# Optimization experiments

Hardware: AMD Instinct MI355X
Metric: run time of the kernel (lower is better)

The kernel has to match this reference:

```python
import jax, jax.numpy as jnp
import numpy as np

N_NODES = 50000
DIM = 128
N_EDGES = 800000
N_UID = 4096
ORDER = 3
LN_EPS = 1e-5


def setup_inputs() -> dict:
    key = jax.random.key(0)
    ks = jax.random.split(key, 6)
    scale = 1.0 / np.sqrt(DIM)
    embedding = jax.random.normal(ks[0], (N_NODES, DIM), jnp.float32) * np.sqrt(2.0 / DIM)  # kaiming-ish
    W = jax.random.normal(ks[1], (ORDER, DIM, DIM), jnp.float32) * scale
    b = jnp.zeros((ORDER, DIM), jnp.float32)
    gamma = jnp.ones((ORDER, DIM), jnp.float32)
    beta = jnp.zeros((ORDER, DIM), jnp.float32)
    src = jax.random.randint(ks[2], (N_EDGES,), 0, N_NODES, jnp.int32)
    dst = jax.random.randint(ks[3], (N_EDGES,), 0, N_NODES, jnp.int32)
    uid = jax.random.randint(ks[4], (N_UID,), 0, N_NODES, jnp.int32)
    return {"embedding": embedding, "W": W, "b": b, "gamma": gamma,
            "beta": beta, "src": src, "dst": dst, "uid": uid}


def _layer_norm(x, g, bta):
    mu = jnp.mean(x, axis=-1, keepdims=True)
    var = jnp.var(x, axis=-1, keepdims=True)
    return (x - mu) * jax.lax.rsqrt(var + LN_EPS) * g + bta


def reference(embedding, W, b, gamma, beta, src, dst, uid):
    # in-degree per destination node (DGL 'gcn' aggregator uses in_degrees)
    deg = jax.ops.segment_sum(jnp.ones((src.shape[0],), embedding.dtype), dst,
                              num_segments=N_NODES)  # [N]
    inv = (1.0 / (deg + 1.0))[:, None]  # [N,1]
    feats = embedding
    for i in range(ORDER):
        # gather source features, scatter-sum into destinations
        neigh = jax.ops.segment_sum(feats[src], dst, num_segments=N_NODES)  # [N,D]
        h = (neigh + feats) * inv                    # gcn-style mean incl. self
        h = jnp.einsum('nd,ed->ne', h, W[i]) + b[i]  # fc_neigh
        feats = jax.nn.elu(_layer_norm(h, gamma[i], beta[i]))
    return feats[uid]  # [N_UID, D]
```

## Files before the change

kernel.cpp:

```cpp
#include <hip/hip_runtime.h>
#include <math.h>

typedef unsigned int   uint;
typedef unsigned short ushort;

#define N_NODES 50000
#define DIM     128
#define N_EDGES 800000
#define N_UID   4096
#define LN_EPS  1e-5f
#define RST     132
#define XST     136
#define NBUCK   196
#define BCAP    4608
#define PCHUNK  4096
#define NCHUNK  ((N_EDGES + PCHUNK - 1) / PCHUNK)

typedef __attribute__((ext_vector_type(8))) short bf16x8;
typedef __attribute__((ext_vector_type(4))) float f32x4;
typedef __attribute__((ext_vector_type(2))) float f32x2;
typedef __attribute__((ext_vector_type(4))) uint  u32x4;

__device__ __forceinline__ float bf_lo(uint u) { return __builtin_bit_cast(float, u << 16); }
__device__ __forceinline__ float bf_hi(uint u) { return __builtin_bit_cast(float, u & 0xffff0000u); }
__device__ __forceinline__ uint pack_bf16(float a, float b) {
    uint ua = __builtin_bit_cast(uint, a);
    uint ub = __builtin_bit_cast(uint, b);
    uint ra = (ua + 0x7fffu + ((ua >> 16) & 1u)) >> 16;
    uint rb = (ub + 0x7fffu + ((ub >> 16) & 1u)) >> 16;
    return ra | (rb << 16);
}

__global__ __launch_bounds__(256) void prep_kernel(const float* __restrict__ emb, ushort* __restrict__ E,
                                                   const float* __restrict__ W, ushort* __restrict__ WB,
                                                   int* __restrict__ bcur,
                                                   ushort* __restrict__ T1, ushort* __restrict__ T2) {
    int i = blockIdx.x * 256 + threadIdx.x;
    if (i < N_NODES * DIM / 4) {
        const float4 v = ((const float4*)emb)[i];
        uint2 p;
        p.x = pack_bf16(v.x, v.y);
        p.y = pack_bf16(v.z, v.w);
        ((uint2*)E)[i] = p;
    }
    if (i < 3 * DIM * DIM / 4) {
        const float4 v = ((const float4*)W)[i];
        uint2 p;
        p.x = pack_bf16(v.x, v.y);
        p.y = pack_bf16(v.z, v.w);
        ((uint2*)WB)[i] = p;
    }
    if (i < 256) bcur[i] = 0;
    if (i < DIM / 4) {
        const uint2 z = make_uint2(0u, 0u);
        ((uint2*)(E  + (size_t)N_NODES * DIM))[i] = z;
        ((uint2*)(T1 + (size_t)N_NODES * DIM))[i] = z;
        ((uint2*)(T2 + (size_t)N_NODES * DIM))[i] = z;
    }
}

__global__ __launch_bounds__(256) void part_kernel(const int* __restrict__ src, const int* __restrict__ dst,
                                                   int* __restrict__ bcur, int* __restrict__ pak) {
    __shared__ int h[256];
    __shared__ int base[256];
    __shared__ int cur[256];
    const int t  = threadIdx.x;
    const int e0 = blockIdx.x * PCHUNK;
    const int e1 = min(e0 + PCHUNK, N_EDGES);
    h[t] = 0;
    __syncthreads();
    for (int i = e0 + t; i < e1; i += 256)
        atomicAdd(&h[dst[i] >> 8], 1);
    __syncthreads();
    if (t < NBUCK && h[t]) base[t] = atomicAdd(&bcur[t], h[t]);
    cur[t] = 0;
    __syncthreads();
    for (int i = e0 + t; i < e1; i += 256) {
        const int s = src[i], d = dst[i];
        const int b = d >> 8;
        const int q = base[b] + atomicAdd(&cur[b], 1);
        if (q < BCAP)
            pak[b * BCAP + q] = (s << 8) | (d & 255);
    }
}

__global__ __launch_bounds__(256) void bucket_kernel(const int* __restrict__ pak, const int* __restrict__ bcur,
                                                     int* __restrict__ off, int* __restrict__ degv,
                                                     int* __restrict__ csr) {
    __shared__ int cnt[256];
    __shared__ int pos[256];
    const int b = blockIdx.x, t = threadIdx.x;
    const int e0 = b * BCAP;
    const int m  = min(bcur[b], BCAP);
    cnt[t] = 0;
    __syncthreads();
    for (int i = t; i < m; i += 256) atomicAdd(&cnt[pak[e0 + i] & 255], 1);
    __syncthreads();
    const int v = cnt[t];
    pos[t] = v;
    __syncthreads();
    for (int o = 1; o < 256; o <<= 1) {
        int x = (t >= o) ? pos[t - o] : 0;
        __syncthreads();
        pos[t] += x;
        __syncthreads();
    }
    const int excl = pos[t] - v;
    const int node = b * 256 + t;
    if (node < N_NODES) { off[node] = e0 + excl; degv[node] = v; }
    __syncthreads();
    pos[t] = excl;
    __syncthreads();
    for (int i = t; i < m; i += 256) {
        const int p = pak[e0 + i];
        const int q = atomicAdd(&pos[p & 255], 1);
        csr[e0 + q] = p >> 8;
    }
}

template <bool OUT_BF16>
__global__ __launch_bounds__(512, 4) void layer_kernel(
    const ushort* __restrict__ fin, void* __restrict__ fout,
    const int* __restrict__ off, const int* __restrict__ degv,
    const int* __restrict__ csr, const int* __restrict__ uidmap,
    const ushort* __restrict__ wb, const float* __restrict__ bias,
    const float* __restrict__ gamma, const float* __restrict__ beta, int nrows)
{
    __shared__ ushort xs[32 * XST];
    __shared__ float  ys[32 * RST];
    const int t = threadIdx.x;
    const int rows = blockIdx.x * 32;

    {
        const int lx   = t & 15;
        const int st   = t >> 4;
        const int slot = rows + st;
        const bool valid = slot < nrows;
        int n = 0;
        if (valid) n = uidmap ? uidmap[slot] : slot;
        const uint4 q0 = ((const uint4*)(fin + (size_t)n * DIM))[lx];
        const int d0 = off[n];
        const int deg = valid ? degv[n] : 0;
        const int d1 = d0 + deg;

        f32x2 a0 = f32x2{bf_lo(q0.x), bf_hi(q0.x)};
        f32x2 a1 = f32x2{bf_lo(q0.y), bf_hi(q0.y)};
        f32x2 a2 = f32x2{bf_lo(q0.z), bf_hi(q0.z)};
        f32x2 a3 = f32x2{bf_lo(q0.w), bf_hi(q0.w)};

        const int rounds = (deg + 7) >> 3;
        int e = d0;
        int ida[8], idb[8];
        uint4 va[8], vb[8];

#define LIDS(ID, BASE) { _Pragma("unroll") for (int k = 0; k < 8; ++k) {        \
            const int ee = (BASE) + k; const int c = csr[ee];                   \
            ID[k] = (ee < d1) ? c : N_NODES; } }
#define LVEC(VV, ID) { _Pragma("unroll") for (int k = 0; k < 8; ++k)            \
            VV[k] = ((const uint4*)(fin + (size_t)ID[k] * DIM))[lx]; }
#define ACC(VV) { _Pragma("unroll") for (int k = 0; k < 8; ++k) {               \
            a0 += f32x2{bf_lo(VV[k].x), bf_hi(VV[k].x)};                        \
            a1 += f32x2{bf_lo(VV[k].y), bf_hi(VV[k].y)};                        \
            a2 += f32x2{bf_lo(VV[k].z), bf_hi(VV[k].z)};                        \
            a3 += f32x2{bf_lo(VV[k].w), bf_hi(VV[k].w)}; } }

        if (rounds > 0) { LIDS(ida, e);     LVEC(va, ida); }
        if (rounds > 1) { LIDS(idb, e + 8); LVEC(vb, idb); }
        for (int r = 0; r < rounds; r += 2) {
            ACC(va);
            if (r + 2 < rounds) { LIDS(ida, e + 16); LVEC(va, ida); }
            if (r + 1 < rounds) {
                ACC(vb);
                if (r + 3 < rounds) { LIDS(idb, e + 24); LVEC(vb, idb); }
            }
            e += 16;
        }
#undef LIDS
#undef LVEC
#undef ACC

        const float iv = 1.0f / (float)(deg + 1);
        uint4 p;
        p.x = pack_bf16(a0.x * iv, a0.y * iv);
        p.y = pack_bf16(a1.x * iv, a1.y * iv);
        p.z = pack_bf16(a2.x * iv, a2.y * iv);
        p.w = pack_bf16(a3.x * iv, a3.y * iv);
        *((uint4*)(xs + st * XST + lx * 8)) = p;
    }
    __syncthreads();

    {
        const int wave = t >> 6, lane = t & 63;
        const int row_off = (wave >> 2) * 16;
        const int col_off = (wave & 3) * 32;
        const int lm   = lane & 15;
        const int quad = lane >> 4;
        f32x4 acc[2] = {f32x4{0,0,0,0}, f32x4{0,0,0,0}};
        const ushort* xrow = xs + (row_off + lm) * XST + quad * 8;
        const ushort* __restrict__ wrow = wb + (size_t)(col_off + lm) * DIM + quad * 8;
        #pragma unroll
        for (int kk = 0; kk < 4; ++kk) {
            const bf16x8 af = __builtin_bit_cast(bf16x8, *(const u32x4*)(xrow + kk * 32));
            #pragma unroll
            for (int c = 0; c < 2; ++c) {
                const bf16x8 bfr = __builtin_bit_cast(bf16x8,
                    *(const u32x4*)(wrow + (size_t)c * 16 * DIM + kk * 32));
                acc[c] = __builtin_amdgcn_mfma_f32_16x16x32_bf16(af, bfr, acc[c], 0, 0, 0);
            }
        }
        #pragma unroll
        for (int c = 0; c < 2; ++c) {
            #pragma unroll
            for (int r = 0; r < 4; ++r)
                ys[(row_off + quad * 4 + r) * RST + col_off + c * 16 + lm] = acc[c][r];
        }
    }
    __syncthreads();

    {
        const int r   = t >> 4;
        const int seg = t & 15;
        const int db  = seg * 8;
        const float* yr = ys + r * RST + db;
        float vs[8];
        {
            const float4 y0 = ((const float4*)yr)[0];
            const float4 y1 = ((const float4*)yr)[1];
            const float4 b0 = ((const float4*)(bias + db))[0];
            const float4 b1 = ((const float4*)(bias + db))[1];
            vs[0] = y0.x + b0.x; vs[1] = y0.y + b0.y; vs[2] = y0.z + b0.z; vs[3] = y0.w + b0.w;
            vs[4] = y1.x + b1.x; vs[5] = y1.y + b1.y; vs[6] = y1.z + b1.z; vs[7] = y1.w + b1.w;
        }
        float s1 = 0.0f, s2 = 0.0f;
        #pragma unroll
        for (int i = 0; i < 8; ++i) { s1 += vs[i]; s2 += vs[i] * vs[i]; }
        #pragma unroll
        for (int m = 1; m < 16; m <<= 1) {
            s1 += __shfl_xor(s1, m);
            s2 += __shfl_xor(s2, m);
        }
        const float mu  = s1 * (1.0f / 128.0f);
        const float var = s2 * (1.0f / 128.0f) - mu * mu;
        const float rs  = rsqrtf(var + LN_EPS);
        float ov[8];
        {
            const float4 g0 = ((const float4*)(gamma + db))[0];
            const float4 g1 = ((const float4*)(gamma + db))[1];
            const float4 t0 = ((const float4*)(beta + db))[0];
            const float4 t1 = ((const float4*)(beta + db))[1];
            float z;
            z = (vs[0] - mu) * rs * g0.x + t0.x; ov[0] = (z > 0.0f) ? z : __expf(z) - 1.0f;
            z = (vs[1] - mu) * rs * g0.y + t0.y; ov[1] = (z > 0.0f) ? z : __expf(z) - 1.0f;
            z = (vs[2] - mu) * rs * g0.z + t0.z; ov[2] = (z > 0.0f) ? z : __expf(z) - 1.0f;
            z = (vs[3] - mu) * rs * g0.w + t0.w; ov[3] = (z > 0.0f) ? z : __expf(z) - 1.0f;
            z = (vs[4] - mu) * rs * g1.x + t1.x; ov[4] = (z > 0.0f) ? z : __expf(z) - 1.0f;
            z = (vs[5] - mu) * rs * g1.y + t1.y; ov[5] = (z > 0.0f) ? z : __expf(z) - 1.0f;
            z = (vs[6] - mu) * rs * g1.z + t1.z; ov[6] = (z > 0.0f) ? z : __expf(z) - 1.0f;
            z = (vs[7] - mu) * rs * g1.w + t1.w; ov[7] = (z > 0.0f) ? z : __expf(z) - 1.0f;
        }
        const int slot = rows + r;
        if (slot < nrows) {
            if (OUT_BF16) {
                uint4 p;
                p.x = pack_bf16(ov[0], ov[1]);
                p.y = pack_bf16(ov[2], ov[3]);
                p.z = pack_bf16(ov[4], ov[5]);
                p.w = pack_bf16(ov[6], ov[7]);
                *((uint4*)((ushort*)fout + (size_t)slot * DIM + db)) = p;
            } else {
                float* op = (float*)fout + (size_t)slot * DIM + db;
                ((float4*)op)[0] = make_float4(ov[0], ov[1], ov[2], ov[3]);
                ((float4*)op)[1] = make_float4(ov[4], ov[5], ov[6], ov[7]);
            }
        }
    }
}

extern "C" void kernel_launch(void* const* d_in, const int* in_sizes, int n_in,
                              void* d_out, int out_size, void* d_ws, size_t ws_size,
                              hipStream_t stream) {
    const float* emb   = (const float*)d_in[0];
    const float* W     = (const float*)d_in[1];
    const float* bias  = (const float*)d_in[2];
    const float* gamma = (const float*)d_in[3];
    const float* beta  = (const float*)d_in[4];
    const int*   src   = (const int*)d_in[5];
    const int*   dst   = (const int*)d_in[6];
    const int*   uid   = (const int*)d_in[7];

    const size_t FROW = (size_t)(N_NODES + 1) * DIM;
    ushort* E    = (ushort*)d_ws;
    ushort* T1   = E + FROW;
    ushort* T2   = T1 + FROW;
    ushort* WB   = T2 + FROW;
    int*    off  = (int*)(WB + 3 * DIM * DIM);
    int*    degv = off + (N_NODES + 4);
    int*    bcur = degv + (N_NODES + 4);
    int*    pak  = bcur + 256;
    int*    csr  = pak + NBUCK * BCAP;

    prep_kernel<<<(N_NODES * DIM / 4 + 255) / 256, 256, 0, stream>>>(emb, E, W, WB, bcur, T1, T2);
    part_kernel<<<NCHUNK, 256, 0, stream>>>(src, dst, bcur, pak);
    bucket_kernel<<<NBUCK, 256, 0, stream>>>(pak, bcur, off, degv, csr);

    const int lblk = (N_NODES + 31) / 32;

    layer_kernel<true><<<lblk, 512, 0, stream>>>(E, T1, off, degv, csr, nullptr, WB,
                                                 bias, gamma, beta, N_NODES);
    layer_kernel<true><<<lblk, 512, 0, stream>>>(T1, T2, off, degv, csr, nullptr, WB + DIM * DIM,
                                                 bias + DIM, gamma + DIM, beta + DIM, N_NODES);
    layer_kernel<false><<<N_UID / 32, 512, 0, stream>>>(T2, (float*)d_out, off, degv, csr, uid,
                                                        WB + 2 * DIM * DIM, bias + 2 * DIM,
                                                        gamma + 2 * DIM, beta + 2 * DIM, N_UID);
}
```

Before: 215.7 us.

## Store node features as per-row 8-bit quantized values with scale/offset metadata

Replaces the bf16 feature tables with uint8 per-row min/max quantization (scale and min kept in a float2 per row). This halves the bytes moved by the random neighbor gather, which dominates the aggregation. Offsets are summed separately and the self row is folded into the gather loop, which now runs with a single-stage prefetch instead of the previous double-buffered one. The cost is a large loss of precision that may exceed tolerance, plus an extra metadata load per neighbor and quantization work in the epilogue.

Result: faster. 209.8 us (-2.7%).

```diff
diff --git a/kernel.cpp b/kernel.cpp
--- a/kernel.cpp
+++ b/kernel.cpp
@@ -3,6 +3,7 @@
 
 typedef unsigned int   uint;
 typedef unsigned short ushort;
+typedef unsigned char  uchar;
 
 #define N_NODES 50000
 #define DIM     128
@@ -15,14 +16,14 @@
 #define BCAP    4608
 #define PCHUNK  4096
 #define NCHUNK  ((N_EDGES + PCHUNK - 1) / PCHUNK)
+#define QBLK    (N_NODES / 16)
+#define WBLK    48
+#define MROW    50004
 
 typedef __attribute__((ext_vector_type(8))) short bf16x8;
 typedef __attribute__((ext_vector_type(4))) float f32x4;
-typedef __attribute__((ext_vector_type(2))) float f32x2;
 typedef __attribute__((ext_vector_type(4))) uint  u32x4;
 
-__device__ __forceinline__ float bf_lo(uint u) { return __builtin_bit_cast(float, u << 16); }
-__device__ __forceinline__ float bf_hi(uint u) { return __builtin_bit_cast(float, u & 0xffff0000u); }
 __device__ __forceinline__ uint pack_bf16(float a, float b) {
     uint ua = __builtin_bit_cast(uint, a);
     uint ub = __builtin_bit_cast(uint, b);
@@ -31,31 +32,52 @@
     return ra | (rb << 16);
 }
 
-__global__ __launch_bounds__(256) void prep_kernel(const float* __restrict__ emb, ushort* __restrict__ E,
+__global__ __launch_bounds__(256) void prep_kernel(const float* __restrict__ emb,
+                                                   uchar* __restrict__ Q0, float2* __restrict__ M0,
                                                    const float* __restrict__ W, ushort* __restrict__ WB,
                                                    int* __restrict__ bcur,
-                                                   ushort* __restrict__ T1, ushort* __restrict__ T2) {
-    int i = blockIdx.x * 256 + threadIdx.x;
-    if (i < N_NODES * DIM / 4) {
-        const float4 v = ((const float4*)emb)[i];
-        uint2 p;
-        p.x = pack_bf16(v.x, v.y);
-        p.y = pack_bf16(v.z, v.w);
-        ((uint2*)E)[i] = p;
-    }
-    if (i < 3 * DIM * DIM / 4) {
+                                                   float2* __restrict__ M1, float2* __restrict__ M2) {
+    const int t = threadIdx.x, b = blockIdx.x;
+    if (b < QBLK) {
+        const int row = b * 16 + (t >> 4);
+        const int seg = t & 15;
+        const float* rp = emb + (size_t)row * DIM + seg * 8;
+        const float4 v0 = ((const float4*)rp)[0];
+        const float4 v1 = ((const float4*)rp)[1];
+        float vs[8] = {v0.x, v0.y, v0.z, v0.w, v1.x, v1.y, v1.z, v1.w};
+        float mn = vs[0], mx = vs[0];
+        #pragma unroll
+        for (int j = 1; j < 8; ++j) { mn = fminf(mn, vs[j]); mx = fmaxf(mx, vs[j]); }
+        #pragma unroll
+        for (int m = 1; m < 16; m <<= 1) {
+            mn = fminf(mn, __shfl_xor(mn, m));
+            mx = fmaxf(mx, __shfl_xor(mx, m));
+        }
+        const float rng = mx - mn;
+        const float rcp = (rng > 0.0f) ? 255.0f / rng : 0.0f;
+        uint bq[8];
+        #pragma unroll
+        for (int j = 0; j < 8; ++j)
+            bq[j] = (uint)fminf(255.0f, fmaf(vs[j] - mn, rcp, 0.5f));
+        uint2 q;
+        q.x = bq[0] | (bq[1] << 8) | (bq[2] << 16) | (bq[3] << 24);
+        q.y = bq[4] | (bq[5] << 8) | (bq[6] << 16) | (bq[7] << 24);
+        ((uint2*)(Q0 + (size_t)row * DIM))[seg] = q;
+        if (seg == 0) M0[row] = make_float2(rng * (1.0f / 255.0f), mn);
+    } else if (b < QBLK + WBLK) {
+        const int i = (b - QBLK) * 256 + t;
         const float4 v = ((const float4*)W)[i];
         uint2 p;
         p.x = pack_bf16(v.x, v.y);
         p.y = pack_bf16(v.z, v.w);
         ((uint2*)WB)[i] = p;
-    }
-    if (i < 256) bcur[i] = 0;
-    if (i < DIM / 4) {
-        const uint2 z = make_uint2(0u, 0u);
-        ((uint2*)(E  + (size_t)N_NODES * DIM))[i] = z;
-        ((uint2*)(T1 + (size_t)N_NODES * DIM))[i] = z;
-        ((uint2*)(T2 + (size_t)N_NODES * DIM))[i] = z;
+    } else {
+        if (t < 256) bcur[t] = 0;
+        if (t == 0) {
+            M0[N_NODES] = make_float2(0.0f, 0.0f);
+            M1[N_NODES] = make_float2(0.0f, 0.0f);
+            M2[N_NODES] = make_float2(0.0f, 0.0f);
+        }
     }
 }
 
@@ -118,9 +140,10 @@
     }
 }
 
-template <bool OUT_BF16>
+template <bool OUT_FP32>
 __global__ __launch_bounds__(512, 4) void layer_kernel(
-    const ushort* __restrict__ fin, void* __restrict__ fout,
+    const uchar* __restrict__ qin, const float2* __restrict__ meta_in,
+    uchar* __restrict__ qout, float2* __restrict__ meta_out, float* __restrict__ fpout,
     const int* __restrict__ off, const int* __restrict__ degv,
     const int* __restrict__ csr, const int* __restrict__ uidmap,
     const ushort* __restrict__ wb, const float* __restrict__ bias,
@@ -138,53 +161,58 @@
         const bool valid = slot < nrows;
         int n = 0;
         if (valid) n = uidmap ? uidmap[slot] : slot;
-        const uint4 q0 = ((const uint4*)(fin + (size_t)n * DIM))[lx];
         const int d0 = off[n];
         const int deg = valid ? degv[n] : 0;
-        const int d1 = d0 + deg;
-
-        f32x2 a0 = f32x2{bf_lo(q0.x), bf_hi(q0.x)};
-        f32x2 a1 = f32x2{bf_lo(q0.y), bf_hi(q0.y)};
-        f32x2 a2 = f32x2{bf_lo(q0.z), bf_hi(q0.z)};
-        f32x2 a3 = f32x2{bf_lo(q0.w), bf_hi(q0.w)};
-
-        const int rounds = (deg + 7) >> 3;
-        int e = d0;
-        int ida[8], idb[8];
-        uint4 va[8], vb[8];
+        const int total = deg + 1;
+
+        float a[8] = {0,0,0,0,0,0,0,0};
+        float O = 0.0f;
+        const int rounds = (total + 7) >> 3;
+        int id[8], idn[8];
+        uint2 qv[8];
+        float2 mt[8];
 
 #define LIDS(ID, BASE) { _Pragma("unroll") for (int k = 0; k < 8; ++k) {        \
-            const int ee = (BASE) + k; const int c = csr[ee];                   \
-            ID[k] = (ee < d1) ? c : N_NODES; } }
-#define LVEC(VV, ID) { _Pragma("unroll") for (int k = 0; k < 8; ++k)            \
-            VV[k] = ((const uint4*)(fin + (size_t)ID[k] * DIM))[lx]; }
-#define ACC(VV) { _Pragma("unroll") for (int k = 0; k < 8; ++k) {               \
-            a0 += f32x2{bf_lo(VV[k].x), bf_hi(VV[k].x)};                        \
-            a1 += f32x2{bf_lo(VV[k].y), bf_hi(VV[k].y)};                        \
-            a2 += f32x2{bf_lo(VV[k].z), bf_hi(VV[k].z)};                        \
-            a3 += f32x2{bf_lo(VV[k].w), bf_hi(VV[k].w)}; } }
-
-        if (rounds > 0) { LIDS(ida, e);     LVEC(va, ida); }
-        if (rounds > 1) { LIDS(idb, e + 8); LVEC(vb, idb); }
-        for (int r = 0; r < rounds; r += 2) {
-            ACC(va);
-            if (r + 2 < rounds) { LIDS(ida, e + 16); LVEC(va, ida); }
-            if (r + 1 < rounds) {
-                ACC(vb);
-                if (r + 3 < rounds) { LIDS(idb, e + 24); LVEC(vb, idb); }
-            }
-            e += 16;
+            const int pos = (BASE) + k;                                         \
+            const int c = csr[d0 + ((pos > 0) ? pos - 1 : 0)];                  \
+            ID[k] = (pos == 0) ? n : ((pos < total) ? c : N_NODES); } }
+
+        LIDS(id, 0);
+        for (int r = 0; r < rounds; ++r) {
+            #pragma unroll
+            for (int k = 0; k < 8; ++k) {
+                qv[k] = ((const uint2*)(qin + (size_t)id[k] * DIM))[lx];
+                mt[k] = meta_in[id[k]];
+            }
+            const bool more = (r + 1 < rounds);
+            if (more) LIDS(idn, (r + 1) * 8);
+            #pragma unroll
+            for (int k = 0; k < 8; ++k) {
+                const float s = mt[k].x;
+                const uint x0 = qv[k].x, x1 = qv[k].y;
+                a[0] = fmaf((float)(x0 & 0xffu),         s, a[0]);
+                a[1] = fmaf((float)((x0 >> 8) & 0xffu),  s, a[1]);
+                a[2] = fmaf((float)((x0 >> 16) & 0xffu), s, a[2]);
+                a[3] = fmaf((float)(x0 >> 24),           s, a[3]);
+                a[4] = fmaf((float)(x1 & 0xffu),         s, a[4]);
+                a[5] = fmaf((float)((x1 >> 8) & 0xffu),  s, a[5]);
+                a[6] = fmaf((float)((x1 >> 16) & 0xffu), s, a[6]);
+                a[7] = fmaf((float)(x1 >> 24),           s, a[7]);
+                O += mt[k].y;
+            }
+            if (more) {
+                #pragma unroll
+                for (int k = 0; k < 8; ++k) id[k] = idn[k];
+            }
         }
 #undef LIDS
-#undef LVEC
-#undef ACC
-
-        const float iv = 1.0f / (float)(deg + 1);
+
+        const float iv = 1.0f / (float)total;
         uint4 p;
-        p.x = pack_bf16(a0.x * iv, a0.y * iv);
-        p.y = pack_bf16(a1.x * iv, a1.y * iv);
-        p.z = pack_bf16(a2.x * iv, a2.y * iv);
-        p.w = pack_bf16(a3.x * iv, a3.y * iv);
+        p.x = pack_bf16((a[0] + O) * iv, (a[1] + O) * iv);
+        p.y = pack_bf16((a[2] + O) * iv, (a[3] + O) * iv);
+        p.z = pack_bf16((a[4] + O) * iv, (a[5] + O) * iv);
+        p.w = pack_bf16((a[6] + O) * iv, (a[7] + O) * iv);
         *((uint4*)(xs + st * XST + lx * 8)) = p;
     }
     __syncthreads();
@@ -259,18 +287,33 @@
             z = (vs[7] - mu) * rs * g1.w + t1.w; ov[7] = (z > 0.0f) ? z : __expf(z) - 1.0f;
         }
         const int slot = rows + r;
-        if (slot < nrows) {
-            if (OUT_BF16) {
-                uint4 p;
-                p.x = pack_bf16(ov[0], ov[1]);
-                p.y = pack_bf16(ov[2], ov[3]);
-                p.z = pack_bf16(ov[4], ov[5]);
-                p.w = pack_bf16(ov[6], ov[7]);
-                *((uint4*)((ushort*)fout + (size_t)slot * DIM + db)) = p;
-            } else {
-                float* op = (float*)fout + (size_t)slot * DIM + db;
+        if (OUT_FP32) {
+            if (slot < nrows) {
+                float* op = fpout + (size_t)slot * DIM + db;
                 ((float4*)op)[0] = make_float4(ov[0], ov[1], ov[2], ov[3]);
                 ((float4*)op)[1] = make_float4(ov[4], ov[5], ov[6], ov[7]);
+            }
+        } else {
+            float mn = ov[0], mx = ov[0];
+            #pragma unroll
+            for (int j = 1; j < 8; ++j) { mn = fminf(mn, ov[j]); mx = fmaxf(mx, ov[j]); }
+            #pragma unroll
+            for (int m = 1; m < 16; m <<= 1) {
+                mn = fminf(mn, __shfl_xor(mn, m));
+                mx = fmaxf(mx, __shfl_xor(mx, m));
+            }
+            if (slot < nrows) {
+                const float rng = mx - mn;
+                const float rcp = (rng > 0.0f) ? 255.0f / rng : 0.0f;
+                uint bq[8];
+                #pragma unroll
+                for (int j = 0; j < 8; ++j)
+                    bq[j] = (uint)fminf(255.0f, fmaf(ov[j] - mn, rcp, 0.5f));
+                uint2 q;
+                q.x = bq[0] | (bq[1] << 8) | (bq[2] << 16) | (bq[3] << 24);
+                q.y = bq[4] | (bq[5] << 8) | (bq[6] << 16) | (bq[7] << 24);
+                ((uint2*)(qout + (size_t)slot * DIM))[seg] = q;
+                if (seg == 0) meta_out[slot] = make_float2(rng * (1.0f / 255.0f), mn);
             }
         }
     }
@@ -288,28 +331,34 @@
     const int*   dst   = (const int*)d_in[6];
     const int*   uid   = (const int*)d_in[7];
 
-    const size_t FROW = (size_t)(N_NODES + 1) * DIM;
-    ushort* E    = (ushort*)d_ws;
-    ushort* T1   = E + FROW;
-    ushort* T2   = T1 + FROW;
-    ushort* WB   = T2 + FROW;
-    int*    off  = (int*)(WB + 3 * DIM * DIM);
+    const size_t QSZ = (size_t)(N_NODES + 1) * DIM;
+    uchar*  Q0  = (uchar*)d_ws;
+    uchar*  Q1  = Q0 + QSZ;
+    uchar*  Q2  = Q1 + QSZ;
+    ushort* WB  = (ushort*)(Q2 + QSZ);
+    float2* M0  = (float2*)(WB + 3 * DIM * DIM);
+    float2* M1  = M0 + MROW;
+    float2* M2  = M1 + MROW;
+    int*    off  = (int*)(M2 + MROW);
     int*    degv = off + (N_NODES + 4);
     int*    bcur = degv + (N_NODES + 4);
     int*    pak  = bcur + 256;
     int*    csr  = pak + NBUCK * BCAP;
 
-    prep_kernel<<<(N_NODES * DIM / 4 + 255) / 256, 256, 0, stream>>>(emb, E, W, WB, bcur, T1, T2);
+    prep_kernel<<<QBLK + WBLK + 1, 256, 0, stream>>>(emb, Q0, M0, W, WB, bcur, M1, M2);
     part_kernel<<<NCHUNK, 256, 0, stream>>>(src, dst, bcur, pak);
     bucket_kernel<<<NBUCK, 256, 0, stream>>>(pak, bcur, off, degv, csr);
 
     const int lblk = (N_NODES + 31) / 32;
 
-    layer_kernel<true><<<lblk, 512, 0, stream>>>(E, T1, off, degv, csr, nullptr, WB,
-                                                 bias, gamma, beta, N_NODES);
-    layer_kernel<true><<<lblk, 512, 0, stream>>>(T1, T2, off, degv, csr, nullptr, WB + DIM * DIM,
-                                                 bias + DIM, gamma + DIM, beta + DIM, N_NODES);
-    layer_kernel<false><<<N_UID / 32, 512, 0, stream>>>(T2, (float*)d_out, off, degv, csr, uid,
-                                                        WB + 2 * DIM * DIM, bias + 2 * DIM,
-                                                        gamma + 2 * DIM, beta + 2 * DIM, N_UID);
-}
+    layer_kernel<false><<<lblk, 512, 0, stream>>>(Q0, M0, Q1, M1, nullptr,
+                                                  off, degv, csr, nullptr, WB,
+                                                  bias, gamma, beta, N_NODES);
+    layer_kernel<false><<<lblk, 512, 0, stream>>>(Q1, M1, Q2, M2, nullptr,
+                                                  off, degv, csr, nullptr, WB + DIM * DIM,
+                                                  bias + DIM, gamma + DIM, beta + DIM, N_NODES);
+    layer_kernel<true><<<N_UID / 32, 512, 0, stream>>>(Q2, M2, nullptr, nullptr, (float*)d_out,
+                                                       off, degv, csr, uid, WB + 2 * DIM * DIM,
+                                                       bias + 2 * DIM, gamma + 2 * DIM,
+                                                       beta + 2 * DIM, N_UID);
+}
```

## Perform neighbor aggregation as segment-mask MFMA over flattened edge list

Applied to the files above, without the earlier changes.

Replaces the per-row vector gather-accumulate with a block-level flattened list of the 32 rows' self and neighbor IDs, built via an in-block prefix sum and binary search. Each wave stages transposed bf16 slices of gathered features in LDS and sums them per segment using MFMA with 0/1 selection masks from a LUT. This balances irregular degrees across the block and moves the accumulation onto matrix cores. It adds LDS staging, extra barriers and setup work, and caps the edges per block at MAXS*32, so high-degree blocks would be truncated.

New measurement: 288.5 us. +33.8%, slower.

```diff
diff --git a/kernel.cpp b/kernel.cpp
--- a/kernel.cpp
+++ b/kernel.cpp
@@ -15,14 +15,13 @@
 #define BCAP    4608
 #define PCHUNK  4096
 #define NCHUNK  ((N_EDGES + PCHUNK - 1) / PCHUNK)
+#define MAXS    28
+#define KST     40
 
 typedef __attribute__((ext_vector_type(8))) short bf16x8;
 typedef __attribute__((ext_vector_type(4))) float f32x4;
-typedef __attribute__((ext_vector_type(2))) float f32x2;
 typedef __attribute__((ext_vector_type(4))) uint  u32x4;
 
-__device__ __forceinline__ float bf_lo(uint u) { return __builtin_bit_cast(float, u << 16); }
-__device__ __forceinline__ float bf_hi(uint u) { return __builtin_bit_cast(float, u & 0xffff0000u); }
 __device__ __forceinline__ uint pack_bf16(float a, float b) {
     uint ua = __builtin_bit_cast(uint, a);
     uint ub = __builtin_bit_cast(uint, b);
@@ -128,64 +127,124 @@
 {
     __shared__ ushort xs[32 * XST];
     __shared__ float  ys[32 * RST];
+    __shared__ ushort stg[8 * 16 * KST];
+    __shared__ int    cum[33];
+    __shared__ int    cntl[32];
+    __shared__ int    narr[32];
+    __shared__ int    doffs[32];
+    __shared__ int    idsl[MAXS * 32];
+    __shared__ uint   mskl[MAXS * 32];
+    __shared__ uint2  lutl[16];
+
     const int t = threadIdx.x;
     const int rows = blockIdx.x * 32;
 
+    if (t < 32) {
+        const int slot = rows + t;
+        int n = 0, dgr = 0, d0o = 0;
+        if (slot < nrows) { n = uidmap ? uidmap[slot] : slot; dgr = degv[n]; d0o = off[n]; }
+        narr[t] = n; doffs[t] = d0o;
+        cntl[t] = (slot < nrows) ? (dgr + 1) : 0;
+    }
+    if (t < 16) {
+        const uint e0 = ((t & 1) ? 0x3F80u : 0u) | ((t & 2) ? 0x3F800000u : 0u);
+        const uint e1 = ((t & 4) ? 0x3F80u : 0u) | ((t & 8) ? 0x3F800000u : 0u);
+        lutl[t] = make_uint2(e0, e1);
+    }
+    __syncthreads();
+    if (t < 32) {
+        int sacc = 0;
+        for (int i = 0; i <= t; ++i) sacc += cntl[i];
+        cum[t + 1] = sacc;
+        if (t == 0) cum[0] = 0;
+    }
+    __syncthreads();
+    const int L = cum[32];
+    const int S = min((L + 31) >> 5, MAXS);
+
+    for (int p = t; p < S * 32; p += 512) {
+        int lo = 0, hi = 32;
+        #pragma unroll
+        for (int it = 0; it < 5; ++it) {
+            const int mid = (lo + hi) >> 1;
+            if (cum[mid] <= p) lo = mid; else hi = mid;
+        }
+        const int i = lo;
+        const int j = p - cum[i];
+        int id = N_NODES;
+        if (p < L) id = (j == 0) ? narr[i] : csr[doffs[i] + j - 1];
+        idsl[p] = id;
+
+        const int i2 = p & 31;
+        const int base = (p >> 5) << 5;
+        const int a = min(max(cum[i2]     - base, 0), 32);
+        const int b = min(max(cum[i2 + 1] - base, 0), 32);
+        const uint mb = (b >= 32) ? 0xFFFFFFFFu : ((1u << b) - 1u);
+        const uint ma = (a >= 32) ? 0xFFFFFFFFu : ((1u << a) - 1u);
+        mskl[p] = mb & ~ma;
+    }
+    __syncthreads();
+
     {
-        const int lx   = t & 15;
-        const int st   = t >> 4;
-        const int slot = rows + st;
-        const bool valid = slot < nrows;
-        int n = 0;
-        if (valid) n = uidmap ? uidmap[slot] : slot;
-        const uint4 q0 = ((const uint4*)(fin + (size_t)n * DIM))[lx];
-        const int d0 = off[n];
-        const int deg = valid ? degv[n] : 0;
-        const int d1 = d0 + deg;
-
-        f32x2 a0 = f32x2{bf_lo(q0.x), bf_hi(q0.x)};
-        f32x2 a1 = f32x2{bf_lo(q0.y), bf_hi(q0.y)};
-        f32x2 a2 = f32x2{bf_lo(q0.z), bf_hi(q0.z)};
-        f32x2 a3 = f32x2{bf_lo(q0.w), bf_hi(q0.w)};
-
-        const int rounds = (deg + 7) >> 3;
-        int e = d0;
-        int ida[8], idb[8];
-        uint4 va[8], vb[8];
-
-#define LIDS(ID, BASE) { _Pragma("unroll") for (int k = 0; k < 8; ++k) {        \
-            const int ee = (BASE) + k; const int c = csr[ee];                   \
-            ID[k] = (ee < d1) ? c : N_NODES; } }
-#define LVEC(VV, ID) { _Pragma("unroll") for (int k = 0; k < 8; ++k)            \
-            VV[k] = ((const uint4*)(fin + (size_t)ID[k] * DIM))[lx]; }
-#define ACC(VV) { _Pragma("unroll") for (int k = 0; k < 8; ++k) {               \
-            a0 += f32x2{bf_lo(VV[k].x), bf_hi(VV[k].x)};                        \
-            a1 += f32x2{bf_lo(VV[k].y), bf_hi(VV[k].y)};                        \
-            a2 += f32x2{bf_lo(VV[k].z), bf_hi(VV[k].z)};                        \
-            a3 += f32x2{bf_lo(VV[k].w), bf_hi(VV[k].w)}; } }
-
-        if (rounds > 0) { LIDS(ida, e);     LVEC(va, ida); }
-        if (rounds > 1) { LIDS(idb, e + 8); LVEC(vb, idb); }
-        for (int r = 0; r < rounds; r += 2) {
-            ACC(va);
-            if (r + 2 < rounds) { LIDS(ida, e + 16); LVEC(va, ida); }
-            if (r + 1 < rounds) {
-                ACC(vb);
-                if (r + 3 < rounds) { LIDS(idb, e + 24); LVEC(vb, idb); }
-            }
-            e += 16;
-        }
-#undef LIDS
-#undef LVEC
-#undef ACC
-
-        const float iv = 1.0f / (float)(deg + 1);
-        uint4 p;
-        p.x = pack_bf16(a0.x * iv, a0.y * iv);
-        p.y = pack_bf16(a1.x * iv, a1.y * iv);
-        p.z = pack_bf16(a2.x * iv, a2.y * iv);
-        p.w = pack_bf16(a3.x * iv, a3.y * iv);
-        *((uint4*)(xs + st * XST + lx * 8)) = p;
+        const int w = t >> 6, l = t & 63;
+        const int kq = l & 7;
+        const int dg = l >> 3;
+        const int goffb = w * 16 + 2 * dg;
+        ushort* sw = stg + w * (16 * KST);
+
+#define LD4(S_, Q_) { \
+            const int bse = (S_) * 32 + 4 * kq; \
+            Q_.x = *(const uint*)(fin + (size_t)idsl[bse + 0] * DIM + goffb); \
+            Q_.y = *(const uint*)(fin + (size_t)idsl[bse + 1] * DIM + goffb); \
+            Q_.z = *(const uint*)(fin + (size_t)idsl[bse + 2] * DIM + goffb); \
+            Q_.w = *(const uint*)(fin + (size_t)idsl[bse + 3] * DIM + goffb); }
+
+        uint4 qa, qb, qc;
+        LD4(0, qa);
+        if (S > 1) { LD4(1, qb); } else qb = qa;
+        if (S > 2) { LD4(2, qc); } else qc = qb;
+
+        const int g = l >> 4, c = l & 15;
+        const int koct = g * 8;
+        const ushort* rp = sw + c * KST + koct;
+        f32x4 acc0 = f32x4{0, 0, 0, 0}, acc1 = f32x4{0, 0, 0, 0};
+
+        for (int s = 0; s < S; ++s) {
+            const uint u0 = (qa.x & 0xffffu) | (qa.y << 16);
+            const uint u1 = (qa.z & 0xffffu) | (qa.w << 16);
+            const uint u2 = (qa.x >> 16)     | (qa.y & 0xffff0000u);
+            const uint u3 = (qa.z >> 16)     | (qa.w & 0xffff0000u);
+            *((uint2*)(sw + (2 * dg)     * KST + 4 * kq)) = make_uint2(u0, u1);
+            *((uint2*)(sw + (2 * dg + 1) * KST + 4 * kq)) = make_uint2(u2, u3);
+            qa = qb; qb = qc;
+            if (s + 3 < S) LD4(s + 3, qc);
+
+            const uint m0 = mskl[s * 32 + c];
+            const uint m1 = mskl[s * 32 + c + 16];
+            const uint b0 = (m0 >> koct) & 0xffu;
+            const uint b1 = (m1 >> koct) & 0xffu;
+            const uint2 p00 = lutl[b0 & 15u], p01 = lutl[b0 >> 4];
+            const uint2 p10 = lutl[b1 & 15u], p11 = lutl[b1 >> 4];
+            const u32x4 a0w = u32x4{p00.x, p00.y, p01.x, p01.y};
+            const u32x4 a1w = u32x4{p10.x, p10.y, p11.x, p11.y};
+
+            const u32x4 bwv = *((const u32x4*)rp);
+            const bf16x8 bfv = __builtin_bit_cast(bf16x8, bwv);
+            acc0 = __builtin_amdgcn_mfma_f32_16x16x32_bf16(__builtin_bit_cast(bf16x8, a0w), bfv, acc0, 0, 0, 0);
+            acc1 = __builtin_amdgcn_mfma_f32_16x16x32_bf16(__builtin_bit_cast(bf16x8, a1w), bfv, acc1, 0, 0, 0);
+        }
+#undef LD4
+
+        const int r0 = g * 4;
+        #pragma unroll
+        for (int r = 0; r < 4; ++r) {
+            const int i0 = r0 + r;
+            const float iv0 = 1.0f / (float)max(cum[i0 + 1] - cum[i0], 1);
+            xs[i0 * XST + w * 16 + c] = (ushort)pack_bf16(acc0[r] * iv0, 0.0f);
+            const int i1 = i0 + 16;
+            const float iv1 = 1.0f / (float)max(cum[i1 + 1] - cum[i1], 1);
+            xs[i1 * XST + w * 16 + c] = (ushort)pack_bf16(acc1[r] * iv1, 0.0f);
+        }
     }
     __syncthreads();
 
@@ -195,24 +254,24 @@
         const int col_off = (wave & 3) * 32;
         const int lm   = lane & 15;
         const int quad = lane >> 4;
-        f32x4 acc[2] = {f32x4{0,0,0,0}, f32x4{0,0,0,0}};
+        f32x4 acc[2] = {f32x4{0, 0, 0, 0}, f32x4{0, 0, 0, 0}};
         const ushort* xrow = xs + (row_off + lm) * XST + quad * 8;
         const ushort* __restrict__ wrow = wb + (size_t)(col_off + lm) * DIM + quad * 8;
         #pragma unroll
         for (int kk = 0; kk < 4; ++kk) {
             const bf16x8 af = __builtin_bit_cast(bf16x8, *(const u32x4*)(xrow + kk * 32));
             #pragma unroll
-            for (int c = 0; c < 2; ++c) {
+            for (int cc = 0; cc < 2; ++cc) {
                 const bf16x8 bfr = __builtin_bit_cast(bf16x8,
-                    *(const u32x4*)(wrow + (size_t)c * 16 * DIM + kk * 32));
-                acc[c] = __builtin_amdgcn_mfma_f32_16x16x32_bf16(af, bfr, acc[c], 0, 0, 0);
+                    *(const u32x4*)(wrow + (size_t)cc * 16 * DIM + kk * 32));
+                acc[cc] = __builtin_amdgcn_mfma_f32_16x16x32_bf16(af, bfr, acc[cc], 0, 0, 0);
             }
         }
         #pragma unroll
-        for (int c = 0; c < 2; ++c) {
+        for (int cc = 0; cc < 2; ++cc) {
             #pragma unroll
             for (int r = 0; r < 4; ++r)
-                ys[(row_off + quad * 4 + r) * RST + col_off + c * 16 + lm] = acc[c][r];
+                ys[(row_off + quad * 4 + r) * RST + col_off + cc * 16 + lm] = acc[cc][r];
         }
     }
     __syncthreads();
```
